# Optimization experiments

Measured on AMD Instinct MI355X. Metric: run time of the kernel, lower is better.

The kernel has to match this reference:

```python
import jax, jax.numpy as jnp
import numpy as np

K = 3  # knnLoss default k


def _knn_loss(source_pc, target_pc, k=K):
    """Faithful translation of knnLoss.forward.

    For each batch: drop exact-zero (0,0,0) points from both clouds
    (emulated via masking for static shapes), find the k nearest *target*
    points for every *source* point (query=source, ref=target), take the
    mean Euclidean distance, then average over batch.
    """

    def per_batch(src, tgt):  # src, tgt: [N, 3]
        src_valid = jnp.any(src != 0.0, axis=-1)  # [Ns] move_zero_point mask
        tgt_valid = jnp.any(tgt != 0.0, axis=-1)  # [Nt]
        s2 = jnp.sum(src * src, axis=-1)          # [Ns]
        t2 = jnp.sum(tgt * tgt, axis=-1)          # [Nt]
        # squared pairwise distances, [Ns, Nt]
        d2 = s2[:, None] + t2[None, :] - 2.0 * (src @ tgt.T)
        d2 = jnp.maximum(d2, 0.0)
        # invalid (zero) target points can never be a neighbor
        d2 = jnp.where(tgt_valid[None, :], d2, jnp.inf)
        neg_top, _ = jax.lax.top_k(-d2, k)        # k smallest squared dists
        dist = jnp.sqrt(-neg_top)                 # [Ns, k] euclidean, like KNN_CUDA
        # mean over valid source points x k neighbors
        num = jnp.sum(jnp.where(src_valid[:, None], dist, 0.0))
        den = jnp.sum(src_valid).astype(dist.dtype) * k
        return num / den

    return jnp.mean(jax.vmap(per_batch)(source_pc, target_pc))


def setup_inputs() -> dict:
    key = jax.random.key(0)
    k1, k2 = jax.random.split(key)
    B, N = 4, 8192
    source_pc = jax.random.normal(k1, (B, N, 3), dtype=jnp.float32)
    target_pc = jax.random.normal(k2, (B, N, 3), dtype=jnp.float32)
    return {"source_pc": source_pc, "target_pc": target_pc}


def reference(source_pc, target_pc):
    return _knn_loss(source_pc, target_pc)
```

## Files before the change

### kernel.cpp

```cpp
#include <hip/hip_runtime.h>
#include <math.h>

#define BATCH 4
#define NPTS 8192
#define TILE 512
#define TSPLIT 16
#define SRC_PER_THREAD 4
#define SRC_PER_BLOCK 1024
#define SRC_CHUNKS 8
#define NSRC_TOT (BATCH * NPTS)

typedef __attribute__((ext_vector_type(2))) float f2;

__device__ __forceinline__ void insert3(float d, float& a0, float& a1, float& a2) {
    float h  = fmaxf(a1, d);
    float m  = __builtin_amdgcn_fmed3f(a0, a1, d);
    a2 = fminf(a2, h);
    a1 = m;
    a0 = fminf(a0, d);
}

__global__ __launch_bounds__(256) void knn_partial(const float* __restrict__ src,
                                                   const float* __restrict__ tgt,
                                                   float* __restrict__ part) {
    __shared__ f2 ts[TILE / 2 * 4];
    const int tid = threadIdx.x;
    const int sc = blockIdx.x, tc = blockIdx.y, b = blockIdx.z;

    {
        const float* tb = tgt + ((size_t)b * NPTS + (size_t)tc * TILE + 2 * tid) * 3;
        float x0 = tb[0], y0 = tb[1], z0 = tb[2];
        float x1 = tb[3], y1 = tb[4], z1 = tb[5];
        float w0 = x0 * x0 + y0 * y0 + z0 * z0;
        float w1 = x1 * x1 + y1 * y1 + z1 * z1;
        if (!(x0 != 0.f || y0 != 0.f || z0 != 0.f)) w0 = 3.0e38f;
        if (!(x1 != 0.f || y1 != 0.f || z1 != 0.f)) w1 = 3.0e38f;
        ts[tid * 4 + 0] = (f2){x0, x1};
        ts[tid * 4 + 1] = (f2){y0, y1};
        ts[tid * 4 + 2] = (f2){z0, z1};
        ts[tid * 4 + 3] = (f2){w0, w1};
    }
    __syncthreads();

    f2 nx[SRC_PER_THREAD], ny[SRC_PER_THREAD], nz[SRC_PER_THREAD], s2[SRC_PER_THREAD];
    #pragma unroll
    for (int s = 0; s < SRC_PER_THREAD; ++s) {
        int i = sc * SRC_PER_BLOCK + tid + 256 * s;
        const float* sp = src + ((size_t)b * NPTS + i) * 3;
        float ax = sp[0], ay = sp[1], az = sp[2];
        float q = ax * ax + ay * ay + az * az;
        nx[s] = (f2){-2.f * ax, -2.f * ax};
        ny[s] = (f2){-2.f * ay, -2.f * ay};
        nz[s] = (f2){-2.f * az, -2.f * az};
        s2[s] = (f2){q, q};
    }

    float e0[SRC_PER_THREAD], e1[SRC_PER_THREAD], e2[SRC_PER_THREAD];
    float o0[SRC_PER_THREAD], o1[SRC_PER_THREAD], o2[SRC_PER_THREAD];
    #pragma unroll
    for (int s = 0; s < SRC_PER_THREAD; ++s) {
        e0[s] = e1[s] = e2[s] = 3e38f;
        o0[s] = o1[s] = o2[s] = 3e38f;
    }

    #pragma unroll 4
    for (int e = 0; e < TILE / 2; ++e) {
        f2 xs = ts[e * 4 + 0];
        f2 ys = ts[e * 4 + 1];
        f2 zs = ts[e * 4 + 2];
        f2 ws = ts[e * 4 + 3];
        #pragma unroll
        for (int s = 0; s < SRC_PER_THREAD; ++s) {
            f2 d = xs * nx[s] + (ys * ny[s] + (zs * nz[s] + (ws + s2[s])));
            insert3(d.x, e0[s], e1[s], e2[s]);
            insert3(d.y, o0[s], o1[s], o2[s]);
        }
    }

    #pragma unroll
    for (int s = 0; s < SRC_PER_THREAD; ++s) {
        insert3(o0[s], e0[s], e1[s], e2[s]);
        insert3(o1[s], e0[s], e1[s], e2[s]);
        insert3(o2[s], e0[s], e1[s], e2[s]);
        size_t flat = (size_t)b * NPTS + sc * SRC_PER_BLOCK + tid + 256 * s;
        part[((size_t)tc * 3 + 0) * NSRC_TOT + flat] = e0[s];
        part[((size_t)tc * 3 + 1) * NSRC_TOT + flat] = e1[s];
        part[((size_t)tc * 3 + 2) * NSRC_TOT + flat] = e2[s];
    }
}

__global__ __launch_bounds__(256) void knn_merge(const float* __restrict__ src,
                                                 const float* __restrict__ part,
                                                 float* __restrict__ acc,
                                                 float* __restrict__ cnt,
                                                 unsigned* __restrict__ ticket,
                                                 float* __restrict__ out) {
    const int gid = blockIdx.x * 256 + threadIdx.x;
    const int b = gid >> 13;

    float m0 = part[0 * NSRC_TOT + gid];
    float m1 = part[1 * NSRC_TOT + gid];
    float m2 = part[2 * NSRC_TOT + gid];
    #pragma unroll
    for (int q = 3; q < TSPLIT * 3; ++q)
        insert3(part[(size_t)q * NSRC_TOT + gid], m0, m1, m2);

    float sx = src[(size_t)gid * 3 + 0];
    float sy = src[(size_t)gid * 3 + 1];
    float sz = src[(size_t)gid * 3 + 2];
    bool valid = (sx != 0.f) || (sy != 0.f) || (sz != 0.f);
    float s = valid ? (sqrtf(fmaxf(m0, 0.f)) + sqrtf(fmaxf(m1, 0.f)) + sqrtf(fmaxf(m2, 0.f)))
                    : 0.f;
    float c = valid ? 1.f : 0.f;

    for (int off = 32; off >= 1; off >>= 1) {
        s += __shfl_down(s, off);
        c += __shfl_down(c, off);
    }
    __shared__ float red_s[4], red_c[4];
    int wave = threadIdx.x >> 6, lane = threadIdx.x & 63;
    if (lane == 0) { red_s[wave] = s; red_c[wave] = c; }
    __syncthreads();
    if (threadIdx.x == 0) {
        float bs = red_s[0] + red_s[1] + red_s[2] + red_s[3];
        float bc = red_c[0] + red_c[1] + red_c[2] + red_c[3];
        atomicAdd(&acc[b], bs);
        atomicAdd(&cnt[b], bc);
        __threadfence();
        unsigned t = atomicAdd(ticket, 1u);
        if (t == (unsigned)(gridDim.x - 1)) {
            float loss = 0.f;
            #pragma unroll
            for (int bb = 0; bb < BATCH; ++bb) {
                float as = atomicAdd(&acc[bb], 0.f);
                float ac = atomicAdd(&cnt[bb], 0.f);
                loss += as / (ac * 3.0f);
            }
            out[0] = loss * (1.0f / BATCH);
        }
    }
}

extern "C" void kernel_launch(void* const* d_in, const int* in_sizes, int n_in,
                              void* d_out, int out_size, void* d_ws, size_t ws_size,
                              hipStream_t stream) {
    const float* src = (const float*)d_in[0];
    const float* tgt = (const float*)d_in[1];
    float* out = (float*)d_out;

    float* acc = (float*)d_ws;
    float* cnt = acc + 4;
    unsigned* ticket = (unsigned*)((char*)d_ws + 32);
    float* part = (float*)((char*)d_ws + 256);

    hipMemsetAsync(d_ws, 0, 256, stream);

    dim3 g1(SRC_CHUNKS, TSPLIT, BATCH);
    knn_partial<<<g1, 256, 0, stream>>>(src, tgt, part);

    knn_merge<<<dim3(NSRC_TOT / 256), 256, 0, stream>>>(src, part, acc, cnt, ticket, out);
}
```

Baseline: 123.5 us.

## Halve sources per thread, merge top-3 lists, drop memset, use float4 LDS

Each thread now handles 2 source points instead of 4, which doubles the grid to raise occupancy. Target tiles are stored as float4 in shared memory so each iteration needs fewer LDS reads, and the distance is built from explicit FMAs. The even/odd lists are combined with a dedicated 3-by-3 merge. The merge kernel splits the 48 partial inserts across four independent chains to shorten the dependency chain. The host memset is removed by zeroing the accumulator header inside the first kernel, at the cost of less source-register reuse per target load.

Measured after the change: 117.3 us. 5.0% less time.

```diff
diff --git a/kernel.cpp b/kernel.cpp
--- a/kernel.cpp
+++ b/kernel.cpp
@@ -5,27 +5,40 @@
 #define NPTS 8192
 #define TILE 512
 #define TSPLIT 16
-#define SRC_PER_THREAD 4
-#define SRC_PER_BLOCK 1024
-#define SRC_CHUNKS 8
+#define SRC_PER_BLOCK 512
+#define SRC_CHUNKS 16
 #define NSRC_TOT (BATCH * NPTS)
 
 typedef __attribute__((ext_vector_type(2))) float f2;
 
 __device__ __forceinline__ void insert3(float d, float& a0, float& a1, float& a2) {
-    float h  = fmaxf(a1, d);
-    float m  = __builtin_amdgcn_fmed3f(a0, a1, d);
+    float h = fmaxf(a1, d);
+    float m = __builtin_amdgcn_fmed3f(a0, a1, d);
     a2 = fminf(a2, h);
     a1 = m;
     a0 = fminf(a0, d);
 }
 
+__device__ __forceinline__ void merge33(float a0, float a1, float a2,
+                                        float& b0, float& b1, float& b2) {
+    float s0 = fminf(a0, b0);
+    float h  = fmaxf(a0, b0);
+    float m  = fminf(a1, b1);
+    float mm = fminf(a2, b2);
+    b1 = fminf(h, m);
+    b2 = __builtin_amdgcn_fmed3f(h, m, mm);
+    b0 = s0;
+}
+
 __global__ __launch_bounds__(256) void knn_partial(const float* __restrict__ src,
                                                    const float* __restrict__ tgt,
-                                                   float* __restrict__ part) {
-    __shared__ f2 ts[TILE / 2 * 4];
+                                                   float* __restrict__ part,
+                                                   float* __restrict__ hdr) {
+    __shared__ float4 ts[TILE / 2 * 2];
     const int tid = threadIdx.x;
     const int sc = blockIdx.x, tc = blockIdx.y, b = blockIdx.z;
+
+    if (sc == 0 && tc == 0 && b == 0 && tid < 16) hdr[tid] = 0.0f;
 
     {
         const float* tb = tgt + ((size_t)b * NPTS + (size_t)tc * TILE + 2 * tid) * 3;
@@ -35,16 +48,14 @@
         float w1 = x1 * x1 + y1 * y1 + z1 * z1;
         if (!(x0 != 0.f || y0 != 0.f || z0 != 0.f)) w0 = 3.0e38f;
         if (!(x1 != 0.f || y1 != 0.f || z1 != 0.f)) w1 = 3.0e38f;
-        ts[tid * 4 + 0] = (f2){x0, x1};
-        ts[tid * 4 + 1] = (f2){y0, y1};
-        ts[tid * 4 + 2] = (f2){z0, z1};
-        ts[tid * 4 + 3] = (f2){w0, w1};
+        ts[2 * tid + 0] = make_float4(x0, x1, y0, y1);
+        ts[2 * tid + 1] = make_float4(z0, z1, w0, w1);
     }
     __syncthreads();
 
-    f2 nx[SRC_PER_THREAD], ny[SRC_PER_THREAD], nz[SRC_PER_THREAD], s2[SRC_PER_THREAD];
+    f2 nx[2], ny[2], nz[2], s2[2];
     #pragma unroll
-    for (int s = 0; s < SRC_PER_THREAD; ++s) {
+    for (int s = 0; s < 2; ++s) {
         int i = sc * SRC_PER_BLOCK + tid + 256 * s;
         const float* sp = src + ((size_t)b * NPTS + i) * 3;
         float ax = sp[0], ay = sp[1], az = sp[2];
@@ -55,37 +66,37 @@
         s2[s] = (f2){q, q};
     }
 
-    float e0[SRC_PER_THREAD], e1[SRC_PER_THREAD], e2[SRC_PER_THREAD];
-    float o0[SRC_PER_THREAD], o1[SRC_PER_THREAD], o2[SRC_PER_THREAD];
+    float c0[2][2], c1[2][2], c2[2][2];
     #pragma unroll
-    for (int s = 0; s < SRC_PER_THREAD; ++s) {
-        e0[s] = e1[s] = e2[s] = 3e38f;
-        o0[s] = o1[s] = o2[s] = 3e38f;
-    }
+    for (int s = 0; s < 2; ++s)
+        for (int h = 0; h < 2; ++h) { c0[s][h] = c1[s][h] = c2[s][h] = 3e38f; }
 
     #pragma unroll 4
     for (int e = 0; e < TILE / 2; ++e) {
-        f2 xs = ts[e * 4 + 0];
-        f2 ys = ts[e * 4 + 1];
-        f2 zs = ts[e * 4 + 2];
-        f2 ws = ts[e * 4 + 3];
+        float4 p = ts[2 * e + 0];
+        float4 q = ts[2 * e + 1];
+        f2 xs = (f2){p.x, p.y};
+        f2 ys = (f2){p.z, p.w};
+        f2 zs = (f2){q.x, q.y};
+        f2 ws = (f2){q.z, q.w};
         #pragma unroll
-        for (int s = 0; s < SRC_PER_THREAD; ++s) {
-            f2 d = xs * nx[s] + (ys * ny[s] + (zs * nz[s] + (ws + s2[s])));
-            insert3(d.x, e0[s], e1[s], e2[s]);
-            insert3(d.y, o0[s], o1[s], o2[s]);
+        for (int s = 0; s < 2; ++s) {
+            f2 acc = ws + s2[s];
+            acc = __builtin_elementwise_fma(zs, nz[s], acc);
+            acc = __builtin_elementwise_fma(ys, ny[s], acc);
+            acc = __builtin_elementwise_fma(xs, nx[s], acc);
+            insert3(acc.x, c0[s][0], c1[s][0], c2[s][0]);
+            insert3(acc.y, c0[s][1], c1[s][1], c2[s][1]);
         }
     }
 
     #pragma unroll
-    for (int s = 0; s < SRC_PER_THREAD; ++s) {
-        insert3(o0[s], e0[s], e1[s], e2[s]);
-        insert3(o1[s], e0[s], e1[s], e2[s]);
-        insert3(o2[s], e0[s], e1[s], e2[s]);
+    for (int s = 0; s < 2; ++s) {
+        merge33(c0[s][1], c1[s][1], c2[s][1], c0[s][0], c1[s][0], c2[s][0]);
         size_t flat = (size_t)b * NPTS + sc * SRC_PER_BLOCK + tid + 256 * s;
-        part[((size_t)tc * 3 + 0) * NSRC_TOT + flat] = e0[s];
-        part[((size_t)tc * 3 + 1) * NSRC_TOT + flat] = e1[s];
-        part[((size_t)tc * 3 + 2) * NSRC_TOT + flat] = e2[s];
+        part[((size_t)tc * 3 + 0) * NSRC_TOT + flat] = c0[s][0];
+        part[((size_t)tc * 3 + 1) * NSRC_TOT + flat] = c1[s][0];
+        part[((size_t)tc * 3 + 2) * NSRC_TOT + flat] = c2[s][0];
     }
 }
 
@@ -98,18 +109,22 @@
     const int gid = blockIdx.x * 256 + threadIdx.x;
     const int b = gid >> 13;
 
-    float m0 = part[0 * NSRC_TOT + gid];
-    float m1 = part[1 * NSRC_TOT + gid];
-    float m2 = part[2 * NSRC_TOT + gid];
+    float t0[4], t1[4], t2[4];
     #pragma unroll
-    for (int q = 3; q < TSPLIT * 3; ++q)
-        insert3(part[(size_t)q * NSRC_TOT + gid], m0, m1, m2);
+    for (int c = 0; c < 4; ++c) { t0[c] = t1[c] = t2[c] = 3e38f; }
+    #pragma unroll
+    for (int q = 0; q < TSPLIT * 3; ++q)
+        insert3(part[(size_t)q * NSRC_TOT + gid], t0[q & 3], t1[q & 3], t2[q & 3]);
+    merge33(t0[1], t1[1], t2[1], t0[0], t1[0], t2[0]);
+    merge33(t0[3], t1[3], t2[3], t0[2], t1[2], t2[2]);
+    merge33(t0[2], t1[2], t2[2], t0[0], t1[0], t2[0]);
 
     float sx = src[(size_t)gid * 3 + 0];
     float sy = src[(size_t)gid * 3 + 1];
     float sz = src[(size_t)gid * 3 + 2];
     bool valid = (sx != 0.f) || (sy != 0.f) || (sz != 0.f);
-    float s = valid ? (sqrtf(fmaxf(m0, 0.f)) + sqrtf(fmaxf(m1, 0.f)) + sqrtf(fmaxf(m2, 0.f)))
+    float s = valid ? (sqrtf(fmaxf(t0[0], 0.f)) + sqrtf(fmaxf(t1[0], 0.f)) +
+                       sqrtf(fmaxf(t2[0], 0.f)))
                     : 0.f;
     float c = valid ? 1.f : 0.f;
 
@@ -122,10 +137,8 @@
     if (lane == 0) { red_s[wave] = s; red_c[wave] = c; }
     __syncthreads();
     if (threadIdx.x == 0) {
-        float bs = red_s[0] + red_s[1] + red_s[2] + red_s[3];
-        float bc = red_c[0] + red_c[1] + red_c[2] + red_c[3];
-        atomicAdd(&acc[b], bs);
-        atomicAdd(&cnt[b], bc);
+        atomicAdd(&acc[b], red_s[0] + red_s[1] + red_s[2] + red_s[3]);
+        atomicAdd(&cnt[b], red_c[0] + red_c[1] + red_c[2] + red_c[3]);
         __threadfence();
         unsigned t = atomicAdd(ticket, 1u);
         if (t == (unsigned)(gridDim.x - 1)) {
@@ -148,15 +161,14 @@
     const float* tgt = (const float*)d_in[1];
     float* out = (float*)d_out;
 
-    float* acc = (float*)d_ws;
-    float* cnt = acc + 4;
+    float* hdr = (float*)d_ws;
+    float* acc = hdr;
+    float* cnt = hdr + 4;
     unsigned* ticket = (unsigned*)((char*)d_ws + 32);
     float* part = (float*)((char*)d_ws + 256);
 
-    hipMemsetAsync(d_ws, 0, 256, stream);
-
     dim3 g1(SRC_CHUNKS, TSPLIT, BATCH);
-    knn_partial<<<g1, 256, 0, stream>>>(src, tgt, part);
+    knn_partial<<<g1, 256, 0, stream>>>(src, tgt, part, hdr);
 
     knn_merge<<<dim3(NSRC_TOT / 256), 256, 0, stream>>>(src, part, acc, cnt, ticket, out);
 }
```
